# Kernel optimization log

Measured on AMD Instinct MI355X. Metric: run time of the kernel, lower is better.

The kernel has to match this reference:

```python
import jax, jax.numpy as jnp
import numpy as np

L, D, H, E, K, HID = 4096, 1024, 16, 8, 2, 4096
HEAD_DIM = D // H
SCALE = 1.0 / np.sqrt(HEAD_DIM)


def setup_inputs() -> dict:
    key = jax.random.key(0)
    ks = jax.random.split(key, 9)
    s = 0.02
    return {
        "Q": jax.random.normal(ks[0], (L, D), dtype=jnp.float32),
        "K": jax.random.normal(ks[1], (L, D), dtype=jnp.float32),
        "V": jax.random.normal(ks[2], (L, D), dtype=jnp.float32),
        "gate_w": jax.random.normal(ks[3], (D, E), dtype=jnp.float32) * s,
        "w1": jax.random.normal(ks[4], (E, D, HID), dtype=jnp.float32) * s,
        "b1": jnp.zeros((E, HID), dtype=jnp.float32),
        "w2": jax.random.normal(ks[5], (E, HID, D), dtype=jnp.float32) * s,
        "b2": jnp.zeros((E, D), dtype=jnp.float32),
    }


def attention(Q, Kt, V):
    # [L, D] -> [L, H, head_dim]
    q = Q.reshape(L, H, HEAD_DIM)
    k = Kt.reshape(L, H, HEAD_DIM)
    v = V.reshape(L, H, HEAD_DIM)
    scores = jnp.einsum("qhd,khd->hqk", q, k) * SCALE  # [H, L, L]
    probs = jax.nn.softmax(scores, axis=-1)
    out = jnp.einsum("hqk,khd->qhd", probs, v)  # [L, H, head_dim]
    return out.reshape(L, D)


def moe(x, gate_w, w1, b1, w2, b2):
    # x: [N, D]; top-k gating with softmax over selected logits
    logits = x @ gate_w  # [N, E]
    topv, topi = jax.lax.top_k(logits, K)  # [N, K]
    topw = jax.nn.softmax(topv, axis=-1)
    rows = jnp.arange(x.shape[0])[:, None]
    full_w = jnp.zeros_like(logits).at[rows, topi].set(topw)  # [N, E]
    # dense-masked expert compute (mathematically identical: zero weights kill
    # unrouted tokens). GELU is exact (erf), matching torch nn.GELU default.
    h = jax.nn.gelu(jnp.einsum("nd,edh->enh", x, w1) + b1[:, None, :],
                    approximate=False)  # [E, N, HID]
    y = jnp.einsum("enh,ehd->end", h, w2) + b2[:, None, :]  # [E, N, D]
    return jnp.einsum("ne,end->nd", full_w, y)  # weighted combine


def reference(Q, K, V, gate_w, w1, b1, w2, b2):
    attn_out = attention(Q, K, V)              # [L, D]
    out = moe(attn_out, gate_w, w1, b1, w2, b2)  # [L, D]
    return out
```

## Files before the change

### kernel.cpp

```cpp
#include <hip/hip_runtime.h>
#include <hip/hip_bf16.h>
#include <math.h>

#define L_SEQ 4096
#define DMODEL 1024
#define NHEAD 16
#define HDIM 64
#define NEXP 8
#define NHID 4096
#define NSLOT (L_SEQ * 2)

typedef __attribute__((ext_vector_type(4))) float f32x4;
typedef __attribute__((ext_vector_type(16))) float f32x16;
typedef __attribute__((ext_vector_type(8))) short s16x8;
typedef __attribute__((ext_vector_type(4))) short s16x4;
typedef __attribute__((ext_vector_type(4))) unsigned u32x4;

__device__ __forceinline__ short f2bf(float f) {
  __hip_bfloat16 h = __float2bfloat16(f);
  return *reinterpret_cast<short*>(&h);
}
__device__ __forceinline__ float bf2f(short s) {
  __hip_bfloat16 h;
  *reinterpret_cast<short*>(&h) = s;
  return __bfloat162float(h);
}
__device__ __forceinline__ void split3(float a, short& h, short& m, short& l) {
  h = f2bf(a);
  float r = a - bf2f(h);
  m = f2bf(r);
  float r2 = r - bf2f(m);
  l = f2bf(r2);
}
__device__ __forceinline__ void gload16(const void* g, void* l) {
  __builtin_amdgcn_global_load_lds(
      (const __attribute__((address_space(1))) void*)g,
      (__attribute__((address_space(3))) void*)l, 16, 0, 0);
}

__global__ __launch_bounds__(256) void split_kernel(const float* __restrict__ src,
                                                    short* __restrict__ hs,
                                                    short* __restrict__ ms,
                                                    short* __restrict__ ls,
                                                    float scale, int nquad) {
  int i = blockIdx.x * 256 + threadIdx.x;
  for (; i < nquad; i += gridDim.x * 256) {
    f32x4 a = reinterpret_cast<const f32x4*>(src)[i];
    a *= scale;
    s16x4 h4, m4, l4;
    #pragma unroll
    for (int j = 0; j < 4; ++j) {
      short h, m, l;
      split3(a[j], h, m, l);
      h4[j] = h; m4[j] = m; l4[j] = l;
    }
    reinterpret_cast<s16x4*>(hs)[i] = h4;
    reinterpret_cast<s16x4*>(ms)[i] = m4;
    reinterpret_cast<s16x4*>(ls)[i] = l4;
  }
}

__global__ __launch_bounds__(256) void split_vt_kernel(const float* __restrict__ V,
                                                       short* __restrict__ Vth,
                                                       short* __restrict__ Vtm,
                                                       short* __restrict__ Vtl) {
  __shared__ float Vlds[64][65];
  const int k0 = blockIdx.x * 64;
  const int head = blockIdx.y;
  const int t = threadIdx.x;
  {
    int r = t >> 2, c = (t & 3) * 16;
    const f32x4* src = reinterpret_cast<const f32x4*>(&V[(size_t)(k0 + r) * DMODEL + head * HDIM + c]);
    #pragma unroll
    for (int j = 0; j < 4; ++j)
      *reinterpret_cast<f32x4*>(&Vlds[r][c + 4 * j]) = src[j];
  }
  __syncthreads();
  {
    int d = t >> 2, kc = (t & 3) * 16;
    s16x8 h8[2], m8[2], l8[2];
    #pragma unroll
    for (int j = 0; j < 16; ++j) {
      float v = Vlds[kc + j][d];
      short h, m, l;
      split3(v, h, m, l);
      h8[j >> 3][j & 7] = h; m8[j >> 3][j & 7] = m; l8[j >> 3][j & 7] = l;
    }
    size_t base = (size_t)(head * HDIM + d) * L_SEQ + k0 + kc;
    *reinterpret_cast<s16x8*>(&Vth[base]) = h8[0];
    *reinterpret_cast<s16x8*>(&Vth[base + 8]) = h8[1];
    *reinterpret_cast<s16x8*>(&Vtm[base]) = m8[0];
    *reinterpret_cast<s16x8*>(&Vtm[base + 8]) = m8[1];
    *reinterpret_cast<s16x8*>(&Vtl[base]) = l8[0];
    *reinterpret_cast<s16x8*>(&Vtl[base + 8]) = l8[1];
  }
}

__global__ __launch_bounds__(256) void wtrans_kernel(const float* __restrict__ src,
                                                     short* __restrict__ dst,
                                                     int R, int C) {
  __shared__ float T[64][65];
  const int e = blockIdx.z;
  const int r0 = blockIdx.y * 64, c0 = blockIdx.x * 64;
  const size_t sbase = (size_t)e * R * C;
  const int t = threadIdx.x;
  {
    int rr = t >> 2, cc = (t & 3) * 16;
    #pragma unroll
    for (int j = 0; j < 4; ++j)
      *reinterpret_cast<f32x4*>(&T[rr][cc + 4 * j]) =
          *reinterpret_cast<const f32x4*>(&src[sbase + (size_t)(r0 + rr) * C + c0 + cc + 4 * j]);
  }
  __syncthreads();
  {
    int c = t >> 2, r = (t & 3) * 16;
    s16x8 v0, v1;
    #pragma unroll
    for (int j = 0; j < 8; ++j) { v0[j] = f2bf(T[r + j][c]); v1[j] = f2bf(T[r + 8 + j][c]); }
    size_t dbase = ((size_t)e * C + c0 + c) * R + r0 + r;
    *reinterpret_cast<s16x8*>(&dst[dbase]) = v0;
    *reinterpret_cast<s16x8*>(&dst[dbase + 8]) = v1;
  }
}

__global__ __launch_bounds__(256, 2) void attn_mfma(
    const short* __restrict__ Qh, const short* __restrict__ Qm, const short* __restrict__ Ql,
    const short* __restrict__ Kh, const short* __restrict__ Km, const short* __restrict__ Kl,
    const short* __restrict__ Vth, const short* __restrict__ Vtm, const short* __restrict__ Vtl,
    float* __restrict__ X) {
  __shared__ short Ks[3][64][70];
  __shared__ short Vs[3][64][70];
  const int lin = blockIdx.x;
  const int swz = (lin & 7) * 64 + (lin >> 3);
  const int head = swz >> 5;
  const int q0 = (swz & 31) << 7;
  const int t = threadIdx.x;
  const int l = t & 63;
  const int wq = t >> 6;
  const int lc = l & 31;
  const int hh = l >> 5;

  const short* Qp[3] = {Qh, Qm, Ql};
  const short* Kp[3] = {Kh, Km, Kl};
  const short* Vp[3] = {Vth, Vtm, Vtl};

  s16x8 qf[3][4];
  {
    size_t qrow = (size_t)(q0 + wq * 32 + lc) * DMODEL + head * HDIM;
    #pragma unroll
    for (int s = 0; s < 3; ++s)
      #pragma unroll
      for (int ds_ = 0; ds_ < 4; ++ds_)
        qf[s][ds_] = *reinterpret_cast<const s16x8*>(&Qp[s][qrow + ds_ * 16 + hh * 8]);
  }

  s16x8 sK[3][2], sV[3][2];
  const int c0 = t * 2;
  const int row0 = c0 >> 3, ch0 = (c0 & 7) * 8;
  const int row1 = (c0 + 1) >> 3, ch1 = ((c0 + 1) & 7) * 8;

  #define LOAD_TILE(k0v)                                                                  \
    _Pragma("unroll")                                                                     \
    for (int s = 0; s < 3; ++s) {                                                         \
      sK[s][0] = *reinterpret_cast<const s16x8*>(&Kp[s][(size_t)((k0v) + row0) * DMODEL + head * HDIM + ch0]); \
      sK[s][1] = *reinterpret_cast<const s16x8*>(&Kp[s][(size_t)((k0v) + row1) * DMODEL + head * HDIM + ch1]); \
      sV[s][0] = *reinterpret_cast<const s16x8*>(&Vp[s][(size_t)(head * HDIM + row0) * L_SEQ + (k0v) + ch0]);  \
      sV[s][1] = *reinterpret_cast<const s16x8*>(&Vp[s][(size_t)(head * HDIM + row1) * L_SEQ + (k0v) + ch1]);  \
    }

  f32x16 acc0 = (f32x16)0.f, acc1 = (f32x16)0.f;
  float l_loc = 0.f;
  const float LOG2E = 1.4426950408889634f;
  const float MBIAS = 46.166241f;

  LOAD_TILE(0);

  for (int kt64 = 0; kt64 < 64; ++kt64) {
    __syncthreads();
    #pragma unroll
    for (int s = 0; s < 3; ++s) {
      *reinterpret_cast<s16x8*>(&Ks[s][row0][ch0]) = sK[s][0];
      *reinterpret_cast<s16x8*>(&Ks[s][row1][ch1]) = sK[s][1];
      *reinterpret_cast<s16x8*>(&Vs[s][row0][ch0]) = sV[s][0];
      *reinterpret_cast<s16x8*>(&Vs[s][row1][ch1]) = sV[s][1];
    }
    __syncthreads();
    if (kt64 < 63) { LOAD_TILE((kt64 + 1) * 64); }

    #pragma unroll
    for (int khalf = 0; khalf < 2; ++khalf) {
      f32x16 st = (f32x16)0.f;
      #pragma unroll
      for (int ds_ = 0; ds_ < 4; ++ds_) {
        s16x8 ah = *reinterpret_cast<const s16x8*>(&Ks[0][khalf * 32 + lc][ds_ * 16 + hh * 8]);
        s16x8 am = *reinterpret_cast<const s16x8*>(&Ks[1][khalf * 32 + lc][ds_ * 16 + hh * 8]);
        s16x8 al = *reinterpret_cast<const s16x8*>(&Ks[2][khalf * 32 + lc][ds_ * 16 + hh * 8]);
        st = __builtin_amdgcn_mfma_f32_32x32x16_bf16(am, qf[1][ds_], st, 0, 0, 0);
        st = __builtin_amdgcn_mfma_f32_32x32x16_bf16(al, qf[0][ds_], st, 0, 0, 0);
        st = __builtin_amdgcn_mfma_f32_32x32x16_bf16(ah, qf[2][ds_], st, 0, 0, 0);
        st = __builtin_amdgcn_mfma_f32_32x32x16_bf16(am, qf[0][ds_], st, 0, 0, 0);
        st = __builtin_amdgcn_mfma_f32_32x32x16_bf16(ah, qf[1][ds_], st, 0, 0, 0);
        st = __builtin_amdgcn_mfma_f32_32x32x16_bf16(ah, qf[0][ds_], st, 0, 0, 0);
      }

      unsigned Eh[4][2], Em[4][2], El[4][2];
      float ps = 0.f;
      #pragma unroll
      for (int q = 0; q < 4; ++q) {
        #pragma unroll
        for (int p = 0; p < 2; ++p) {
          float a = exp2f(fmaf(st[4 * q + 2 * p],     LOG2E, -MBIAS));
          float b = exp2f(fmaf(st[4 * q + 2 * p + 1], LOG2E, -MBIAS));
          ps += a + b;
          unsigned ua = __float_as_uint(a), ub = __float_as_uint(b);
          unsigned ha = ua & 0xffff0000u, hb = ub & 0xffff0000u;
          Eh[q][p] = (ha >> 16) | hb;
          float ra = a - __uint_as_float(ha), rb = b - __uint_as_float(hb);
          unsigned ma = __float_as_uint(ra) & 0xffff0000u, mb = __float_as_uint(rb) & 0xffff0000u;
          Em[q][p] = (ma >> 16) | mb;
          float la = ra - __uint_as_float(ma), lb = rb - __uint_as_float(mb);
          El[q][p] = ((__float_as_uint(la) & 0xffff0000u) >> 16) | (__float_as_uint(lb) & 0xffff0000u);
        }
      }
      l_loc += ps;

      #define EXCH(E, Fout) do { u32x4 f_;                                        \
        _Pragma("unroll") for (int p_ = 0; p_ < 2; ++p_) {                        \
          unsigned sel_ = hh ? E[2 * ks][p_] : E[2 * ks + 1][p_];                 \
          unsigned rc_ = (unsigned)__shfl_xor((int)sel_, 32);                     \
          f_[p_] = hh ? rc_ : E[2 * ks][p_];                                      \
          f_[2 + p_] = hh ? E[2 * ks + 1][p_] : rc_;                              \
        }                                                                         \
        Fout = *reinterpret_cast<s16x8*>(&f_); } while (0)

      #pragma unroll
      for (int ks = 0; ks < 2; ++ks) {
        s16x8 Fh, Fm, Fl;
        EXCH(Eh, Fh);
        EXCH(Em, Fm);
        EXCH(El, Fl);
        const int kcol = khalf * 32 + ks * 16 + hh * 8;
        {
          s16x8 vh = *reinterpret_cast<const s16x8*>(&Vs[0][lc][kcol]);
          s16x8 vm = *reinterpret_cast<const s16x8*>(&Vs[1][lc][kcol]);
          s16x8 vl = *reinterpret_cast<const s16x8*>(&Vs[2][lc][kcol]);
          acc0 = __builtin_amdgcn_mfma_f32_32x32x16_bf16(Fm, vm, acc0, 0, 0, 0);
          acc0 = __builtin_amdgcn_mfma_f32_32x32x16_bf16(Fl, vh, acc0, 0, 0, 0);
          acc0 = __builtin_amdgcn_mfma_f32_32x32x16_bf16(Fh, vl, acc0, 0, 0, 0);
          acc0 = __builtin_amdgcn_mfma_f32_32x32x16_bf16(Fm, vh, acc0, 0, 0, 0);
          acc0 = __builtin_amdgcn_mfma_f32_32x32x16_bf16(Fh, vm, acc0, 0, 0, 0);
          acc0 = __builtin_amdgcn_mfma_f32_32x32x16_bf16(Fh, vh, acc0, 0, 0, 0);
        }
        {
          s16x8 vh = *reinterpret_cast<const s16x8*>(&Vs[0][32 + lc][kcol]);
          s16x8 vm = *reinterpret_cast<const s16x8*>(&Vs[1][32 + lc][kcol]);
          s16x8 vl = *reinterpret_cast<const s16x8*>(&Vs[2][32 + lc][kcol]);
          acc1 = __builtin_amdgcn_mfma_f32_32x32x16_bf16(Fm, vm, acc1, 0, 0, 0);
          acc1 = __builtin_amdgcn_mfma_f32_32x32x16_bf16(Fl, vh, acc1, 0, 0, 0);
          acc1 = __builtin_amdgcn_mfma_f32_32x32x16_bf16(Fh, vl, acc1, 0, 0, 0);
          acc1 = __builtin_amdgcn_mfma_f32_32x32x16_bf16(Fm, vh, acc1, 0, 0, 0);
          acc1 = __builtin_amdgcn_mfma_f32_32x32x16_bf16(Fh, vm, acc1, 0, 0, 0);
          acc1 = __builtin_amdgcn_mfma_f32_32x32x16_bf16(Fh, vh, acc1, 0, 0, 0);
        }
      }
      #undef EXCH
    }
  }

  float l_tot = l_loc + __shfl_xor(l_loc, 32);
  float inv = 1.f / l_tot;
  #pragma unroll
  for (int r = 0; r < 16; ++r) {
    int qrow_ = (r & 3) + 8 * (r >> 2) + 4 * hh;
    float invr = __int_as_float(__builtin_amdgcn_ds_bpermute(qrow_ << 2, __float_as_int(inv)));
    size_t base = (size_t)(q0 + wq * 32 + qrow_) * DMODEL + head * HDIM + lc;
    X[base] = acc0[r] * invr;
    X[base + 32] = acc1[r] * invr;
  }
}

__global__ __launch_bounds__(256) void tobf16_kernel(const float* __restrict__ src,
                                                     short* __restrict__ dst, int n8) {
  int i = blockIdx.x * 256 + threadIdx.x;
  if (i >= n8) return;
  const f32x4* s = reinterpret_cast<const f32x4*>(src) + (size_t)i * 2;
  f32x4 a = s[0], b = s[1];
  s16x8 r;
  #pragma unroll
  for (int j = 0; j < 4; ++j) { r[j] = f2bf(a[j]); r[4 + j] = f2bf(b[j]); }
  reinterpret_cast<s16x8*>(dst)[i] = r;
}

__global__ __launch_bounds__(256) void gate_kernel(const float* __restrict__ X,
                                                   const float* __restrict__ GW,
                                                   int* __restrict__ tokE,
                                                   float* __restrict__ tokW,
                                                   int* __restrict__ meta) {
  const int gid = blockIdx.x * 256 + threadIdx.x;
  const int n = gid >> 6;
  const int lane = threadIdx.x & 63;
  double lacc[8];
  #pragma unroll
  for (int e = 0; e < 8; ++e) lacc[e] = 0.0;
  #pragma unroll
  for (int ch = 0; ch < 4; ++ch) {
    int d0 = ch * 256 + lane * 4;
    f32x4 xv = *reinterpret_cast<const f32x4*>(&X[(size_t)n * DMODEL + d0]);
    #pragma unroll
    for (int j = 0; j < 4; ++j) {
      const f32x4* g = reinterpret_cast<const f32x4*>(&GW[(size_t)(d0 + j) * 8]);
      f32x4 g0 = g[0], g1 = g[1];
      double xd = (double)xv[j];
      lacc[0] += xd * (double)g0[0]; lacc[1] += xd * (double)g0[1];
      lacc[2] += xd * (double)g0[2]; lacc[3] += xd * (double)g0[3];
      lacc[4] += xd * (double)g1[0]; lacc[5] += xd * (double)g1[1];
      lacc[6] += xd * (double)g1[2]; lacc[7] += xd * (double)g1[3];
    }
  }
  #pragma unroll
  for (int e = 0; e < 8; ++e) {
    double v = lacc[e];
    #pragma unroll
    for (int off = 32; off > 0; off >>= 1) v += __shfl_down(v, off);
    lacc[e] = v;
  }
  if (lane == 0) {
    float lg[8];
    #pragma unroll
    for (int e = 0; e < 8; ++e) lg[e] = (float)lacc[e];
    int i0 = 0;
    for (int e = 1; e < 8; ++e) if (lg[e] > lg[i0]) i0 = e;
    int i1 = -1;
    for (int e = 0; e < 8; ++e) {
      if (e == i0) continue;
      if (i1 < 0 || lg[e] > lg[i1]) i1 = e;
    }
    float eb = expf(lg[i1] - lg[i0]);
    float wa = 1.f / (1.f + eb);
    float wb = eb * wa;
    tokE[2 * n] = i0; tokE[2 * n + 1] = i1;
    tokW[2 * n] = wa; tokW[2 * n + 1] = wb;
    atomicAdd(&meta[i0], 1);
    atomicAdd(&meta[i1], 1);
  }
}

__global__ void scan_kernel(int* meta) {
  if (threadIdx.x == 0) {
    int s = 0;
    for (int e = 0; e < 8; ++e) { meta[8 + e] = s; meta[16 + e] = s; s += meta[e]; }
  }
}

__global__ __launch_bounds__(256) void assign_kernel(const int* __restrict__ tokE,
                                                     const float* __restrict__ tokW,
                                                     int* __restrict__ meta,
                                                     int* __restrict__ list,
                                                     float* __restrict__ wl) {
  int n = blockIdx.x * 256 + threadIdx.x;
  if (n >= L_SEQ) return;
  #pragma unroll
  for (int k2 = 0; k2 < 2; ++k2) {
    int e = tokE[2 * n + k2];
    int slot = atomicAdd(&meta[16 + e], 1);
    list[slot] = n;
    wl[slot] = tokW[2 * n + k2];
  }
}

__global__ __launch_bounds__(256) void gemm1p_kernel(const short* __restrict__ Xb,
                                                     const short* __restrict__ W1t,
                                                     const float* __restrict__ B1,
                                                     const int* __restrict__ meta,
                                                     const int* __restrict__ list,
                                                     short* __restrict__ Hb) {
  const int e = blockIdx.z;
  const int cntE = meta[e];
  const int flat = blockIdx.x + gridDim.x * blockIdx.y;
  const int xcd = flat & 7;
  const int idx = flat >> 3;
  const int m0 = (idx & 31) << 7;
  const int n0 = ((xcd << 2) + (idx >> 5)) << 7;
  if (m0 >= cntE) return;
  const int baseE = meta[8 + e];

  __shared__ short As[2][128 * 64];
  __shared__ short Bs[2][128 * 64];

  const int t = threadIdx.x;
  const int l = t & 63;
  const int w = t >> 6;
  const int wm = w >> 1, wn = w & 1;
  const int ln = l & 15, kg = l >> 4;

  size_t asrc[4], bsrc[4];
  #pragma unroll
  for (int c = 0; c < 4; ++c) {
    int row = c * 32 + w * 8 + (l >> 3);
    int idxm = m0 + row; if (idxm > cntE - 1) idxm = cntE - 1;
    int grow = list[baseE + idxm];
    int sch = (l & 7) ^ (row & 7);
    asrc[c] = ((size_t)grow * DMODEL + sch * 8) * 2;
    bsrc[c] = (((size_t)e * NHID + n0 + row) * DMODEL + sch * 8) * 2;
  }

  f32x4 acc[4][4];
  #pragma unroll
  for (int mi = 0; mi < 4; ++mi)
    #pragma unroll
    for (int ni = 0; ni < 4; ++ni) acc[mi][ni] = (f32x4)0.f;

  #define STAGE1(buf, ktv) do {                                                     \
    size_t koff = (size_t)(ktv) * 128;                                              \
    _Pragma("unroll")                                                               \
    for (int c = 0; c < 4; ++c) {                                                   \
      gload16((const char*)Xb + asrc[c] + koff, (char*)As + (buf) * 16384 + c * 4096 + w * 1024);  \
      gload16((const char*)W1t + bsrc[c] + koff, (char*)Bs + (buf) * 16384 + c * 4096 + w * 1024); \
    } } while (0)

  STAGE1(0, 0);
  __syncthreads();
  int cur = 0;
  for (int kt = 0; kt < 16; ++kt) {
    if (kt < 15) STAGE1(cur ^ 1, kt + 1);
    #pragma unroll
    for (int dc = 0; dc < 2; ++dc) {
      s16x8 af[4];
      #pragma unroll
      for (int mi = 0; mi < 4; ++mi) {
        int row = wm * 64 + mi * 16 + ln;
        int c = (dc * 4 + kg) ^ (row & 7);
        af[mi] = *reinterpret_cast<const s16x8*>((char*)As + cur * 16384 + row * 128 + c * 16);
      }
      #pragma unroll
      for (int ni = 0; ni < 4; ++ni) {
        int col = wn * 64 + ni * 16 + ln;
        int c = (dc * 4 + kg) ^ (col & 7);
        s16x8 bfr = *reinterpret_cast<const s16x8*>((char*)Bs + cur * 16384 + col * 128 + c * 16);
        #pragma unroll
        for (int mi = 0; mi < 4; ++mi)
          acc[mi][ni] = __builtin_amdgcn_mfma_f32_16x16x32_bf16(af[mi], bfr, acc[mi][ni], 0, 0, 0);
      }
    }
    __syncthreads();
    cur ^= 1;
  }

  #pragma unroll
  for (int mi = 0; mi < 4; ++mi) {
    #pragma unroll
    for (int r = 0; r < 4; ++r) {
      int rl = wm * 64 + mi * 16 + kg * 4 + r;
      if (m0 + rl >= cntE) continue;
      size_t hrow = (size_t)(baseE + m0 + rl) * NHID;
      #pragma unroll
      for (int ni = 0; ni < 4; ++ni) {
        int col = n0 + wn * 64 + ni * 16 + ln;
        float z = acc[mi][ni][r] + B1[e * NHID + col];
        float g = 0.5f * z * (1.f + erff(z * 0.70710678118f));
        Hb[hrow + col] = f2bf(g);
      }
    }
  }
}

__global__ __launch_bounds__(256) void gemm2p_kernel(const short* __restrict__ Hb,
                                                     const short* __restrict__ W2t,
                                                     const float* __restrict__ B2,
                                                     const int* __restrict__ meta,
                                                     const int* __restrict__ list,
                                                     const float* __restrict__ wl,
                                                     float* __restrict__ out) {
  const int e = blockIdx.z;
  const int cntE = meta[e];
  const int flat = blockIdx.x + gridDim.x * blockIdx.y;
  const int m0 = (flat >> 3) << 7;
  const int n0 = (flat & 7) << 7;
  if (m0 >= cntE) return;
  const int baseE = meta[8 + e];

  __shared__ short As[2][128 * 64];
  __shared__ short Bs[2][128 * 64];

  const int t = threadIdx.x;
  const int l = t & 63;
  const int w = t >> 6;
  const int wm = w >> 1, wn = w & 1;
  const int ln = l & 15, kg = l >> 4;

  size_t asrc[4], bsrc[4];
  #pragma unroll
  for (int c = 0; c < 4; ++c) {
    int row = c * 32 + w * 8 + (l >> 3);
    int idxm = m0 + row; if (idxm > cntE - 1) idxm = cntE - 1;
    int sch = (l & 7) ^ (row & 7);
    asrc[c] = (((size_t)(baseE + idxm)) * NHID + sch * 8) * 2;
    bsrc[c] = (((size_t)e * DMODEL + n0 + row) * NHID + sch * 8) * 2;
  }

  f32x4 acc[4][4];
  #pragma unroll
  for (int mi = 0; mi < 4; ++mi)
    #pragma unroll
    for (int ni = 0; ni < 4; ++ni) acc[mi][ni] = (f32x4)0.f;

  #define STAGE2(buf, ktv) do {                                                     \
    size_t koff = (size_t)(ktv) * 128;                                              \
    _Pragma("unroll")                                                               \
    for (int c = 0; c < 4; ++c) {                                                   \
      gload16((const char*)Hb + asrc[c] + koff, (char*)As + (buf) * 16384 + c * 4096 + w * 1024);  \
      gload16((const char*)W2t + bsrc[c] + koff, (char*)Bs + (buf) * 16384 + c * 4096 + w * 1024); \
    } } while (0)

  STAGE2(0, 0);
  __syncthreads();
  int cur = 0;
  for (int kt = 0; kt < 64; ++kt) {
    if (kt < 63) STAGE2(cur ^ 1, kt + 1);
    #pragma unroll
    for (int dc = 0; dc < 2; ++dc) {
      s16x8 af[4];
      #pragma unroll
      for (int mi = 0; mi < 4; ++mi) {
        int row = wm * 64 + mi * 16 + ln;
        int c = (dc * 4 + kg) ^ (row & 7);
        af[mi] = *reinterpret_cast<const s16x8*>((char*)As + cur * 16384 + row * 128 + c * 16);
      }
      #pragma unroll
      for (int ni = 0; ni < 4; ++ni) {
        int col = wn * 64 + ni * 16 + ln;
        int c = (dc * 4 + kg) ^ (col & 7);
        s16x8 bfr = *reinterpret_cast<const s16x8*>((char*)Bs + cur * 16384 + col * 128 + c * 16);
        #pragma unroll
        for (int mi = 0; mi < 4; ++mi)
          acc[mi][ni] = __builtin_amdgcn_mfma_f32_16x16x32_bf16(af[mi], bfr, acc[mi][ni], 0, 0, 0);
      }
    }
    __syncthreads();
    cur ^= 1;
  }

  #pragma unroll
  for (int mi = 0; mi < 4; ++mi) {
    #pragma unroll
    for (int r = 0; r < 4; ++r) {
      int rl = wm * 64 + mi * 16 + kg * 4 + r;
      if (m0 + rl >= cntE) continue;
      int slot = baseE + m0 + rl;
      int token = list[slot];
      float wgt = wl[slot];
      #pragma unroll
      for (int ni = 0; ni < 4; ++ni) {
        int col = n0 + wn * 64 + ni * 16 + ln;
        float z = acc[mi][ni][r] + B2[e * DMODEL + col];
        atomicAdd(&out[(size_t)token * DMODEL + col], wgt * z);
      }
    }
  }
}

extern "C" void kernel_launch(void* const* d_in, const int* in_sizes, int n_in,
                              void* d_out, int out_size, void* d_ws, size_t ws_size,
                              hipStream_t stream) {
  const float* Q  = (const float*)d_in[0];
  const float* K  = (const float*)d_in[1];
  const float* V  = (const float*)d_in[2];
  const float* GW = (const float*)d_in[3];
  const float* W1 = (const float*)d_in[4];
  const float* B1 = (const float*)d_in[5];
  const float* W2 = (const float*)d_in[6];
  const float* B2 = (const float*)d_in[7];
  float* out = (float*)d_out;

  const size_t SPLIT = (size_t)L_SEQ * DMODEL;
  const size_t WT_BYTES = (size_t)NEXP * NHID * DMODEL * 2;
  const size_t SPLIT_REGION = SPLIT * 2 * 9;
  const size_t SMALL = (size_t)L_SEQ * 2 * 4 * 2 + (size_t)NSLOT * 4 * 2 + 256;
  const size_t PRIMARY_BYTES = WT_BYTES * 2 + SPLIT_REGION + SPLIT * 4 + SMALL;
  if (ws_size < PRIMARY_BYTES) return;

  char* ws = (char*)d_ws;
  const int nquad = (int)(SPLIT / 4);

  size_t off = 0;
  short* W1t = (short*)(ws + off); off += WT_BYTES;
  short* W2t = (short*)(ws + off); off += WT_BYTES;
  char*  splits = ws + off;        off += SPLIT_REGION;
  short* Qh = (short*)(splits);
  short* Qm = Qh + SPLIT;  short* Ql = Qm + SPLIT;
  short* Kh = Ql + SPLIT;  short* Km = Kh + SPLIT;  short* Kl = Km + SPLIT;
  short* Vth = Kl + SPLIT; short* Vtm = Vth + SPLIT; short* Vtl = Vtm + SPLIT;
  short* Hb = (short*)splits;
  short* Xb = (short*)(splits + (size_t)NSLOT * NHID * 2);
  float* Xf = (float*)(ws + off);  off += SPLIT * 4;
  int*   tokE = (int*)(ws + off);  off += (size_t)L_SEQ * 2 * 4;
  float* tokW = (float*)(ws + off); off += (size_t)L_SEQ * 2 * 4;
  int*   list = (int*)(ws + off);  off += (size_t)NSLOT * 4;
  float* wl = (float*)(ws + off);  off += (size_t)NSLOT * 4;
  int*   meta = (int*)(ws + off);  off += 256;

  hipMemsetAsync(out, 0, (size_t)out_size * sizeof(float), stream);
  hipMemsetAsync(meta, 0, 256, stream);

  wtrans_kernel<<<dim3(64, 16, 8), 256, 0, stream>>>(W1, W1t, DMODEL, NHID);
  wtrans_kernel<<<dim3(16, 64, 8), 256, 0, stream>>>(W2, W2t, NHID, DMODEL);
  split_kernel<<<dim3(2048), 256, 0, stream>>>(Q, Qh, Qm, Ql, 0.125f, nquad);
  split_kernel<<<dim3(2048), 256, 0, stream>>>(K, Kh, Km, Kl, 1.0f, nquad);
  split_vt_kernel<<<dim3(64, 16), 256, 0, stream>>>(V, Vth, Vtm, Vtl);
  attn_mfma<<<dim3(512), 256, 0, stream>>>(Qh, Qm, Ql, Kh, Km, Kl, Vth, Vtm, Vtl, Xf);
  tobf16_kernel<<<dim3(2048), 256, 0, stream>>>(Xf, Xb, (int)(SPLIT / 8));
  gate_kernel<<<dim3(1024), 256, 0, stream>>>(Xf, GW, tokE, tokW, meta);
  scan_kernel<<<1, 64, 0, stream>>>(meta);
  assign_kernel<<<dim3(16), 256, 0, stream>>>(tokE, tokW, meta, list, wl);
  gemm1p_kernel<<<dim3(32, 32, 8), 256, 0, stream>>>(Xb, W1t, B1, meta, list, Hb);
  gemm2p_kernel<<<dim3(32, 8, 8), 256, 0, stream>>>(Hb, W2t, B2, meta, list, wl, out);
}
```

Baseline: 1.069 ms.

## Triple-buffer MoE GEMM K-loop and fuse bf16 cast into attention epilogue

Both expert GEMM kernels switch from a double-buffered 64-wide K tile with __syncthreads to a triple-buffered 32-wide K tile. They use explicit vmcnt waits and a single barrier per step so that two tiles of loads stay in flight, and the LDS swizzle is changed to suit the narrower rows. Separately, the attention epilogue now writes the bf16 copy of its output directly, which removes the tobf16 kernel launch and its extra read of the float activations. The trade-offs are twice as many loop iterations with smaller MFMA batches per barrier, and scattered 2-byte stores in the attention epilogue.

```diff
diff --git a/kernel.cpp b/kernel.cpp
--- a/kernel.cpp
+++ b/kernel.cpp
@@ -127,7 +127,7 @@
     const short* __restrict__ Qh, const short* __restrict__ Qm, const short* __restrict__ Ql,
     const short* __restrict__ Kh, const short* __restrict__ Km, const short* __restrict__ Kl,
     const short* __restrict__ Vth, const short* __restrict__ Vtm, const short* __restrict__ Vtl,
-    float* __restrict__ X) {
+    float* __restrict__ X, short* __restrict__ Xb) {
   __shared__ short Ks[3][64][70];
   __shared__ short Vs[3][64][70];
   const int lin = blockIdx.x;
@@ -274,21 +274,12 @@
     int qrow_ = (r & 3) + 8 * (r >> 2) + 4 * hh;
     float invr = __int_as_float(__builtin_amdgcn_ds_bpermute(qrow_ << 2, __float_as_int(inv)));
     size_t base = (size_t)(q0 + wq * 32 + qrow_) * DMODEL + head * HDIM + lc;
-    X[base] = acc0[r] * invr;
-    X[base + 32] = acc1[r] * invr;
-  }
-}
-
-__global__ __launch_bounds__(256) void tobf16_kernel(const float* __restrict__ src,
-                                                     short* __restrict__ dst, int n8) {
-  int i = blockIdx.x * 256 + threadIdx.x;
-  if (i >= n8) return;
-  const f32x4* s = reinterpret_cast<const f32x4*>(src) + (size_t)i * 2;
-  f32x4 a = s[0], b = s[1];
-  s16x8 r;
-  #pragma unroll
-  for (int j = 0; j < 4; ++j) { r[j] = f2bf(a[j]); r[4 + j] = f2bf(b[j]); }
-  reinterpret_cast<s16x8*>(dst)[i] = r;
+    float o0 = acc0[r] * invr, o1 = acc1[r] * invr;
+    X[base] = o0;
+    X[base + 32] = o1;
+    Xb[base] = f2bf(o0);
+    Xb[base + 32] = f2bf(o1);
+  }
 }
 
 __global__ __launch_bounds__(256) void gate_kernel(const float* __restrict__ X,
@@ -384,8 +375,8 @@
   if (m0 >= cntE) return;
   const int baseE = meta[8 + e];
 
-  __shared__ short As[2][128 * 64];
-  __shared__ short Bs[2][128 * 64];
+  __shared__ short As[3][128 * 32];
+  __shared__ short Bs[3][128 * 32];
 
   const int t = threadIdx.x;
   const int l = t & 63;
@@ -393,13 +384,14 @@
   const int wm = w >> 1, wn = w & 1;
   const int ln = l & 15, kg = l >> 4;
 
-  size_t asrc[4], bsrc[4];
-  #pragma unroll
-  for (int c = 0; c < 4; ++c) {
-    int row = c * 32 + w * 8 + (l >> 3);
+  size_t asrc[2], bsrc[2];
+  #pragma unroll
+  for (int c = 0; c < 2; ++c) {
+    int idx2 = c * 256 + t;
+    int row = idx2 >> 2;
+    int sch = (idx2 & 3) ^ ((row >> 2) & 3);
     int idxm = m0 + row; if (idxm > cntE - 1) idxm = cntE - 1;
     int grow = list[baseE + idxm];
-    int sch = (l & 7) ^ (row & 7);
     asrc[c] = ((size_t)grow * DMODEL + sch * 8) * 2;
     bsrc[c] = (((size_t)e * NHID + n0 + row) * DMODEL + sch * 8) * 2;
   }
@@ -410,40 +402,37 @@
     #pragma unroll
     for (int ni = 0; ni < 4; ++ni) acc[mi][ni] = (f32x4)0.f;
 
-  #define STAGE1(buf, ktv) do {                                                     \
-    size_t koff = (size_t)(ktv) * 128;                                              \
+  #define STG1(h_, bf_) do { size_t ko_ = (size_t)(h_) * 64;                        \
     _Pragma("unroll")                                                               \
-    for (int c = 0; c < 4; ++c) {                                                   \
-      gload16((const char*)Xb + asrc[c] + koff, (char*)As + (buf) * 16384 + c * 4096 + w * 1024);  \
-      gload16((const char*)W1t + bsrc[c] + koff, (char*)Bs + (buf) * 16384 + c * 4096 + w * 1024); \
+    for (int c_ = 0; c_ < 2; ++c_) {                                                \
+      gload16((const char*)Xb + asrc[c_] + ko_, (char*)As + (bf_) * 8192 + c_ * 4096 + t * 16);  \
+      gload16((const char*)W1t + bsrc[c_] + ko_, (char*)Bs + (bf_) * 8192 + c_ * 4096 + t * 16); \
     } } while (0)
 
-  STAGE1(0, 0);
-  __syncthreads();
-  int cur = 0;
-  for (int kt = 0; kt < 16; ++kt) {
-    if (kt < 15) STAGE1(cur ^ 1, kt + 1);
-    #pragma unroll
-    for (int dc = 0; dc < 2; ++dc) {
-      s16x8 af[4];
-      #pragma unroll
-      for (int mi = 0; mi < 4; ++mi) {
-        int row = wm * 64 + mi * 16 + ln;
-        int c = (dc * 4 + kg) ^ (row & 7);
-        af[mi] = *reinterpret_cast<const s16x8*>((char*)As + cur * 16384 + row * 128 + c * 16);
-      }
-      #pragma unroll
-      for (int ni = 0; ni < 4; ++ni) {
-        int col = wn * 64 + ni * 16 + ln;
-        int c = (dc * 4 + kg) ^ (col & 7);
-        s16x8 bfr = *reinterpret_cast<const s16x8*>((char*)Bs + cur * 16384 + col * 128 + c * 16);
-        #pragma unroll
-        for (int mi = 0; mi < 4; ++mi)
-          acc[mi][ni] = __builtin_amdgcn_mfma_f32_16x16x32_bf16(af[mi], bfr, acc[mi][ni], 0, 0, 0);
-      }
-    }
-    __syncthreads();
-    cur ^= 1;
+  const int H = DMODEL / 32;
+  STG1(0, 0); STG1(1, 1);
+  for (int h = 0; h < H; ++h) {
+    if (h < H - 1) asm volatile("s_waitcnt vmcnt(4)\ns_barrier" ::: "memory");
+    else           asm volatile("s_waitcnt vmcnt(0)\ns_barrier" ::: "memory");
+    if (h + 2 < H) STG1(h + 2, (h + 2) % 3);
+    const char* ab = (const char*)As + (h % 3) * 8192;
+    const char* bb = (const char*)Bs + (h % 3) * 8192;
+    s16x8 af[4];
+    #pragma unroll
+    for (int mi = 0; mi < 4; ++mi) {
+      int row = wm * 64 + mi * 16 + ln;
+      int cc = kg ^ ((row >> 2) & 3);
+      af[mi] = *reinterpret_cast<const s16x8*>(ab + row * 64 + cc * 16);
+    }
+    #pragma unroll
+    for (int ni = 0; ni < 4; ++ni) {
+      int col = wn * 64 + ni * 16 + ln;
+      int cc = kg ^ ((col >> 2) & 3);
+      s16x8 bfr = *reinterpret_cast<const s16x8*>(bb + col * 64 + cc * 16);
+      #pragma unroll
+      for (int mi = 0; mi < 4; ++mi)
+        acc[mi][ni] = __builtin_amdgcn_mfma_f32_16x16x32_bf16(af[mi], bfr, acc[mi][ni], 0, 0, 0);
+    }
   }
 
   #pragma unroll
@@ -479,8 +468,8 @@
   if (m0 >= cntE) return;
   const int baseE = meta[8 + e];
 
-  __shared__ short As[2][128 * 64];
-  __shared__ short Bs[2][128 * 64];
+  __shared__ short As[3][128 * 32];
+  __shared__ short Bs[3][128 * 32];
 
   const int t = threadIdx.x;
   const int l = t & 63;
@@ -488,12 +477,13 @@
   const int wm = w >> 1, wn = w & 1;
   const int ln = l & 15, kg = l >> 4;
 
-  size_t asrc[4], bsrc[4];
-  #pragma unroll
-  for (int c = 0; c < 4; ++c) {
-    int row = c * 32 + w * 8 + (l >> 3);
+  size_t asrc[2], bsrc[2];
+  #pragma unroll
+  for (int c = 0; c < 2; ++c) {
+    int idx2 = c * 256 + t;
+    int row = idx2 >> 2;
+    int sch = (idx2 & 3) ^ ((row >> 2) & 3);
     int idxm = m0 + row; if (idxm > cntE - 1) idxm = cntE - 1;
-    int sch = (l & 7) ^ (row & 7);
     asrc[c] = (((size_t)(baseE + idxm)) * NHID + sch * 8) * 2;
     bsrc[c] = (((size_t)e * DMODEL + n0 + row) * NHID + sch * 8) * 2;
   }
@@ -504,40 +494,37 @@
     #pragma unroll
     for (int ni = 0; ni < 4; ++ni) acc[mi][ni] = (f32x4)0.f;
 
-  #define STAGE2(buf, ktv) do {                                                     \
-    size_t koff = (size_t)(ktv) * 128;                                              \
+  #define STG2(h_, bf_) do { size_t ko_ = (size_t)(h_) * 64;                        \
     _Pragma("unroll")                                                               \
-    for (int c = 0; c < 4; ++c) {                                                   \
-      gload16((const char*)Hb + asrc[c] + koff, (char*)As + (buf) * 16384 + c * 4096 + w * 1024);  \
-      gload16((const char*)W2t + bsrc[c] + koff, (char*)Bs + (buf) * 16384 + c * 4096 + w * 1024); \
+    for (int c_ = 0; c_ < 2; ++c_) {                                                \
+      gload16((const char*)Hb + asrc[c_] + ko_, (char*)As + (bf_) * 8192 + c_ * 4096 + t * 16);  \
+      gload16((const char*)W2t + bsrc[c_] + ko_, (char*)Bs + (bf_) * 8192 + c_ * 4096 + t * 16); \
     } } while (0)
 
-  STAGE2(0, 0);
-  __syncthreads();
-  int cur = 0;
-  for (int kt = 0; kt < 64; ++kt) {
-    if (kt < 63) STAGE2(cur ^ 1, kt + 1);
-    #pragma unroll
-    for (int dc = 0; dc < 2; ++dc) {
-      s16x8 af[4];
-      #pragma unroll
-      for (int mi = 0; mi < 4; ++mi) {
-        int row = wm * 64 + mi * 16 + ln;
-        int c = (dc * 4 + kg) ^ (row & 7);
-        af[mi] = *reinterpret_cast<const s16x8*>((char*)As + cur * 16384 + row * 128 + c * 16);
-      }
-      #pragma unroll
-      for (int ni = 0; ni < 4; ++ni) {
-        int col = wn * 64 + ni * 16 + ln;
-        int c = (dc * 4 + kg) ^ (col & 7);
-        s16x8 bfr = *reinterpret_cast<const s16x8*>((char*)Bs + cur * 16384 + col * 128 + c * 16);
-        #pragma unroll
-        for (int mi = 0; mi < 4; ++mi)
-          acc[mi][ni] = __builtin_amdgcn_mfma_f32_16x16x32_bf16(af[mi], bfr, acc[mi][ni], 0, 0, 0);
-      }
-    }
-    __syncthreads();
-    cur ^= 1;
+  const int H = NHID / 32;
+  STG2(0, 0); STG2(1, 1);
+  for (int h = 0; h < H; ++h) {
+    if (h < H - 1) asm volatile("s_waitcnt vmcnt(4)\ns_barrier" ::: "memory");
+    else           asm volatile("s_waitcnt vmcnt(0)\ns_barrier" ::: "memory");
+    if (h + 2 < H) STG2(h + 2, (h + 2) % 3);
+    const char* ab = (const char*)As + (h % 3) * 8192;
+    const char* bb = (const char*)Bs + (h % 3) * 8192;
+    s16x8 af[4];
+    #pragma unroll
+    for (int mi = 0; mi < 4; ++mi) {
+      int row = wm * 64 + mi * 16 + ln;
+      int cc = kg ^ ((row >> 2) & 3);
+      af[mi] = *reinterpret_cast<const s16x8*>(ab + row * 64 + cc * 16);
+    }
+    #pragma unroll
+    for (int ni = 0; ni < 4; ++ni) {
+      int col = wn * 64 + ni * 16 + ln;
+      int cc = kg ^ ((col >> 2) & 3);
+      s16x8 bfr = *reinterpret_cast<const s16x8*>(bb + col * 64 + cc * 16);
+      #pragma unroll
+      for (int mi = 0; mi < 4; ++mi)
+        acc[mi][ni] = __builtin_amdgcn_mfma_f32_16x16x32_bf16(af[mi], bfr, acc[mi][ni], 0, 0, 0);
+    }
   }
 
   #pragma unroll
@@ -576,7 +563,7 @@
   const size_t WT_BYTES = (size_t)NEXP * NHID * DMODEL * 2;
   const size_t SPLIT_REGION = SPLIT * 2 * 9;
   const size_t SMALL = (size_t)L_SEQ * 2 * 4 * 2 + (size_t)NSLOT * 4 * 2 + 256;
-  const size_t PRIMARY_BYTES = WT_BYTES * 2 + SPLIT_REGION + SPLIT * 4 + SMALL;
+  const size_t PRIMARY_BYTES = WT_BYTES * 2 + SPLIT_REGION + SPLIT * 4 + SPLIT * 2 + SMALL;
   if (ws_size < PRIMARY_BYTES) return;
 
   char* ws = (char*)d_ws;
@@ -591,8 +578,8 @@
   short* Kh = Ql + SPLIT;  short* Km = Kh + SPLIT;  short* Kl = Km + SPLIT;
   short* Vth = Kl + SPLIT; short* Vtm = Vth + SPLIT; short* Vtl = Vtm + SPLIT;
   short* Hb = (short*)splits;
-  short* Xb = (short*)(splits + (size_t)NSLOT * NHID * 2);
   float* Xf = (float*)(ws + off);  off += SPLIT * 4;
+  short* Xb = (short*)(ws + off);  off += SPLIT * 2;
   int*   tokE = (int*)(ws + off);  off += (size_t)L_SEQ * 2 * 4;
   float* tokW = (float*)(ws + off); off += (size_t)L_SEQ * 2 * 4;
   int*   list = (int*)(ws + off);  off += (size_t)NSLOT * 4;
@@ -607,8 +594,7 @@
   split_kernel<<<dim3(2048), 256, 0, stream>>>(Q, Qh, Qm, Ql, 0.125f, nquad);
   split_kernel<<<dim3(2048), 256, 0, stream>>>(K, Kh, Km, Kl, 1.0f, nquad);
   split_vt_kernel<<<dim3(64, 16), 256, 0, stream>>>(V, Vth, Vtm, Vtl);
-  attn_mfma<<<dim3(512), 256, 0, stream>>>(Qh, Qm, Ql, Kh, Km, Kl, Vth, Vtm, Vtl, Xf);
-  tobf16_kernel<<<dim3(2048), 256, 0, stream>>>(Xf, Xb, (int)(SPLIT / 8));
+  attn_mfma<<<dim3(512), 256, 0, stream>>>(Qh, Qm, Ql, Kh, Km, Kl, Vth, Vtm, Vtl, Xf, Xb);
   gate_kernel<<<dim3(1024), 256, 0, stream>>>(Xf, GW, tokE, tokW, meta);
   scan_kernel<<<1, 64, 0, stream>>>(meta);
   assign_kernel<<<dim3(16), 256, 0, stream>>>(tokE, tokW, meta, list, wl);
```

Measured after the change: 992.3 us. 7.2% less time.
